# Optimization experiments

Hardware: AMD Instinct MI355X
Metric: run time of the kernel (lower is better)

The kernel has to match this reference:

```python
import jax, jax.numpy as jnp
import numpy as np

HIDDEN = 1024
N_EXPERTS = 16
TOP_K = 2
D_FF_EXPERT = 512
D_FF_SHARED = 2048
BATCH, SEQ = 1, 4096


def setup_inputs() -> dict:
    key = jax.random.key(0)
    ks = jax.random.split(key, 8)
    s = 0.02  # init scale to keep router logits sane
    return {
        "x": jax.random.normal(ks[0], (BATCH, SEQ, HIDDEN), dtype=jnp.float32),
        "router_w": jax.random.normal(ks[1], (HIDDEN, N_EXPERTS), dtype=jnp.float32) * s,
        "experts_gate": jax.random.normal(ks[2], (N_EXPERTS, HIDDEN, D_FF_EXPERT), dtype=jnp.float32) * s,
        "experts_up": jax.random.normal(ks[3], (N_EXPERTS, HIDDEN, D_FF_EXPERT), dtype=jnp.float32) * s,
        "experts_down": jax.random.normal(ks[4], (N_EXPERTS, D_FF_EXPERT, HIDDEN), dtype=jnp.float32) * s,
        "shared_gate": jax.random.normal(ks[5], (HIDDEN, D_FF_SHARED), dtype=jnp.float32) * s,
        "shared_up": jax.random.normal(ks[6], (HIDDEN, D_FF_SHARED), dtype=jnp.float32) * s,
        "shared_down": jax.random.normal(ks[7], (D_FF_SHARED, HIDDEN), dtype=jnp.float32) * s,
    }


def reference(x, router_w, experts_gate, experts_up, experts_down,
              shared_gate, shared_up, shared_down):
    B, S, D = x.shape
    T = B * S
    E = experts_gate.shape[0]

    # Shared SwiGLU expert on all tokens: silu(x@Wg) * (x@Wu) @ Wd
    shared_out = (jax.nn.silu(x @ shared_gate) * (x @ shared_up)) @ shared_down  # [B,S,D]

    x_flat = x.reshape(T, D)
    router_probs = jax.nn.softmax(x_flat @ router_w, axis=-1)          # [T,E]
    topk_w, topk_idx = jax.lax.top_k(router_probs, TOP_K)              # [T,k]

    # Combine weights as dense [T,E]; top-k indices are distinct per token,
    # exactly reproducing sum_{i in topk} w_i * expert_i(x).
    combine = jnp.zeros((T, E), x.dtype).at[jnp.arange(T)[:, None], topk_idx].add(topk_w)

    # Per-expert SwiGLU, vectorized over the (small, fixed) expert axis.
    gate = jnp.einsum('td,edf->etf', x_flat, experts_gate)             # [E,T,f]
    up = jnp.einsum('td,edf->etf', x_flat, experts_up)                 # [E,T,f]
    inter = jax.nn.silu(gate) * up                                     # [E,T,f]
    routed = jnp.einsum('etf,efd,te->td', inter, experts_down, combine)  # [T,D]

    return (shared_out.reshape(T, D) + routed).reshape(B, S, D)
```

## Files before the change

kernel.cpp:

```cpp
#include <hip/hip_runtime.h>
#include <hip/hip_bf16.h>
#include <stdint.h>

#define HIDDEN 1024
#define NEXP 16
#define DFF_E 512
#define DFF_S 2048
#define TOKENS 4096
#define NSLOTS 8192

typedef __bf16 bf16x8 __attribute__((ext_vector_type(8)));
typedef float f32x4 __attribute__((ext_vector_type(4)));

__device__ __forceinline__ unsigned short f2bf(float f) {
  unsigned int u = __builtin_bit_cast(unsigned int, f);
  u += 0x7FFFu + ((u >> 16) & 1u);
  return (unsigned short)(u >> 16);
}
__device__ __forceinline__ float bf2f(unsigned short h) {
  unsigned int u = ((unsigned int)h) << 16;
  return __builtin_bit_cast(float, u);
}
__device__ __forceinline__ void gload16(const void* g, void* l) {
  __builtin_amdgcn_global_load_lds(
      (const __attribute__((address_space(1))) unsigned int*)g,
      (__attribute__((address_space(3))) unsigned int*)l, 16, 0, 0);
}

__global__ void router_kernel(const float* __restrict__ x, const float* __restrict__ rw,
                              int* __restrict__ topk_idx, float* __restrict__ topk_w,
                              int* __restrict__ counts) {
  const int t = blockIdx.x;
  const int lane = threadIdx.x;
  float acc[NEXP];
#pragma unroll
  for (int e = 0; e < NEXP; e++) acc[e] = 0.f;
  const float* xr = x + (size_t)t * HIDDEN;
  for (int d = lane; d < HIDDEN; d += 64) {
    const float xv = xr[d];
    const float4* r = (const float4*)(rw + (size_t)d * NEXP);
#pragma unroll
    for (int q = 0; q < 4; q++) {
      float4 rv = r[q];
      acc[q * 4 + 0] += xv * rv.x;
      acc[q * 4 + 1] += xv * rv.y;
      acc[q * 4 + 2] += xv * rv.z;
      acc[q * 4 + 3] += xv * rv.w;
    }
  }
#pragma unroll
  for (int off = 32; off >= 1; off >>= 1)
#pragma unroll
    for (int e = 0; e < NEXP; e++) acc[e] += __shfl_xor(acc[e], off);

  if (lane == 0) {
    float m = acc[0];
#pragma unroll
    for (int e = 1; e < NEXP; e++) m = fmaxf(m, acc[e]);
    float p[NEXP];
    float s = 0.f;
#pragma unroll
    for (int e = 0; e < NEXP; e++) { p[e] = __expf(acc[e] - m); s += p[e]; }
    const float inv = 1.f / s;
    int i0 = 0; float p0 = p[0];
#pragma unroll
    for (int e = 1; e < NEXP; e++) if (p[e] > p0) { p0 = p[e]; i0 = e; }
    int i1 = -1; float p1 = -1.f;
#pragma unroll
    for (int e = 0; e < NEXP; e++) if (e != i0 && p[e] > p1) { p1 = p[e]; i1 = e; }
    topk_idx[t * 2 + 0] = i0;
    topk_idx[t * 2 + 1] = i1;
    topk_w[t * 2 + 0] = p0 * inv;
    topk_w[t * 2 + 1] = p1 * inv;
    atomicAdd(&counts[i0], 1);
    atomicAdd(&counts[i1], 1);
  }
}

__global__ void offsets_kernel(const int* __restrict__ counts, int* __restrict__ offs,
                               int* __restrict__ cursors) {
  if (threadIdx.x == 0) {
    int run = 0;
    for (int e = 0; e < NEXP; e++) { offs[e] = run; run += counts[e]; }
    offs[NEXP] = run;
  }
  if (threadIdx.x < NEXP) cursors[threadIdx.x] = 0;
}

__global__ void build_slots_kernel(const int* __restrict__ topk_idx, const float* __restrict__ topk_w,
                                   const int* __restrict__ offs, int* __restrict__ cursors,
                                   int* __restrict__ slot_token, float* __restrict__ slot_w,
                                   int* __restrict__ slot_pos) {
  const int t = blockIdx.x * blockDim.x + threadIdx.x;
  if (t >= TOKENS) return;
#pragma unroll
  for (int i = 0; i < 2; i++) {
    const int e = topk_idx[t * 2 + i];
    const int pos = atomicAdd(&cursors[e], 1);
    const int slot = offs[e] + pos;
    slot_token[slot] = t;
    slot_w[slot] = topk_w[t * 2 + i];
    slot_pos[t * 2 + i] = slot;
  }
}

__global__ void convert_kernel(const float* __restrict__ in, unsigned short* __restrict__ out, int n) {
  const int i = (blockIdx.x * blockDim.x + threadIdx.x) * 4;
  if (i >= n) return;
  const float4 v = *(const float4*)(in + i);
  ushort4 o;
  o.x = f2bf(v.x); o.y = f2bf(v.y); o.z = f2bf(v.z); o.w = f2bf(v.w);
  *(ushort4*)(out + i) = o;
}

__global__ void transpose_convert_kernel(const float* __restrict__ in, unsigned short* __restrict__ out,
                                         int K, int N) {
  __shared__ float tile[32][33];
  const int b = blockIdx.z;
  const int k0 = blockIdx.x * 32, n0 = blockIdx.y * 32;
  const float* src = in + (size_t)b * K * N;
  unsigned short* dst = out + (size_t)b * K * N;
  const int tx = threadIdx.x & 31, ty = threadIdx.x >> 5;
#pragma unroll
  for (int r = 0; r < 32; r += 8)
    tile[ty + r][tx] = src[(size_t)(k0 + ty + r) * N + n0 + tx];
  __syncthreads();
#pragma unroll
  for (int r = 0; r < 32; r += 8)
    dst[(size_t)(n0 + ty + r) * K + k0 + tx] = f2bf(tile[tx][ty + r]);
}

template <int GATHER>
__global__ __launch_bounds__(256) void fused_gu_k(const unsigned short* __restrict__ A,
                                                  const unsigned short* __restrict__ Bg,
                                                  const unsigned short* __restrict__ Bu,
                                                  unsigned short* __restrict__ C,
                                                  int M, int N, int K,
                                                  const int* __restrict__ offs,
                                                  const int* __restrict__ slot_token,
                                                  const float* __restrict__ slot_w) {
  __shared__ __align__(16) unsigned short As[128 * 32];
  __shared__ __align__(16) unsigned short Bgs[128 * 32];
  __shared__ __align__(16) unsigned short Bus[128 * 32];
  const int tid = threadIdx.x;
  const int lane = tid & 63;
  const int wid = tid >> 6;
  const int wr = wid >> 1, wc = wid & 1;
  const int fr = lane & 15, fq = lane >> 4;

  int rowBase, rowEnd;
  const unsigned short* Bgp = Bg;
  const unsigned short* Bup = Bu;
  if constexpr (GATHER) {
    const int e = blockIdx.z;
    const int o0 = offs[e], o1 = offs[e + 1];
    rowBase = o0 + blockIdx.x * 128;
    if (rowBase >= o1) return;
    rowEnd = o1;
    Bgp += (size_t)e * (size_t)N * (size_t)K;
    Bup += (size_t)e * (size_t)N * (size_t)K;
  } else {
    rowBase = blockIdx.x * 128;
    rowEnd = M;
  }
  const int colBase = blockIdx.y * 128;

  const int rA = tid >> 2;
  const int kOff = (tid & 3) * 8;
  const unsigned short *aRow0, *aRow1;
  {
    const int r0 = rowBase + rA, r1 = rowBase + rA + 64;
    if constexpr (GATHER) {
      const int s0 = r0 < NSLOTS ? r0 : NSLOTS - 1;
      const int s1 = r1 < NSLOTS ? r1 : NSLOTS - 1;
      aRow0 = A + (size_t)slot_token[s0] * (size_t)K;
      aRow1 = A + (size_t)slot_token[s1] * (size_t)K;
    } else {
      const int m0 = r0 < M ? r0 : M - 1;
      const int m1 = r1 < M ? r1 : M - 1;
      aRow0 = A + (size_t)m0 * (size_t)K;
      aRow1 = A + (size_t)m1 * (size_t)K;
    }
  }
  const unsigned short* bgRow0 = Bgp + (size_t)(colBase + rA) * (size_t)K;
  const unsigned short* bgRow1 = Bgp + (size_t)(colBase + rA + 64) * (size_t)K;
  const unsigned short* buRow0 = Bup + (size_t)(colBase + rA) * (size_t)K;
  const unsigned short* buRow1 = Bup + (size_t)(colBase + rA + 64) * (size_t)K;

  f32x4 accg[4][4], accu[4][4];
#pragma unroll
  for (int i = 0; i < 4; i++)
#pragma unroll
    for (int j = 0; j < 4; j++) {
      accg[i][j] = (f32x4){0.f, 0.f, 0.f, 0.f};
      accu[i][j] = (f32x4){0.f, 0.f, 0.f, 0.f};
    }

  const unsigned short* AsR = As + (wr * 64 + fr) * 32 + fq * 8;
  const unsigned short* BgsR = Bgs + (wc * 64 + fr) * 32 + fq * 8;
  const unsigned short* BusR = Bus + (wc * 64 + fr) * 32 + fq * 8;

  for (int k0 = 0; k0 < K; k0 += 32) {
    __syncthreads();
    gload16(aRow0 + k0 + kOff, As + tid * 8);
    gload16(aRow1 + k0 + kOff, As + 2048 + tid * 8);
    gload16(bgRow0 + k0 + kOff, Bgs + tid * 8);
    gload16(bgRow1 + k0 + kOff, Bgs + 2048 + tid * 8);
    gload16(buRow0 + k0 + kOff, Bus + tid * 8);
    gload16(buRow1 + k0 + kOff, Bus + 2048 + tid * 8);
    __syncthreads();
    bf16x8 af[4], bgf[4], buf[4];
#pragma unroll
    for (int m = 0; m < 4; m++) af[m] = *(const bf16x8*)(AsR + m * 512);
#pragma unroll
    for (int n = 0; n < 4; n++) bgf[n] = *(const bf16x8*)(BgsR + n * 512);
#pragma unroll
    for (int n = 0; n < 4; n++) buf[n] = *(const bf16x8*)(BusR + n * 512);
#pragma unroll
    for (int m = 0; m < 4; m++)
#pragma unroll
      for (int n = 0; n < 4; n++) {
        accg[m][n] = __builtin_amdgcn_mfma_f32_16x16x32_bf16(af[m], bgf[n], accg[m][n], 0, 0, 0);
        accu[m][n] = __builtin_amdgcn_mfma_f32_16x16x32_bf16(af[m], buf[n], accu[m][n], 0, 0, 0);
      }
  }

#pragma unroll
  for (int m = 0; m < 4; m++) {
    const int rb = rowBase + wr * 64 + m * 16 + fq * 4;
#pragma unroll
    for (int n = 0; n < 4; n++) {
      const int col = colBase + wc * 64 + n * 16 + fr;
#pragma unroll
      for (int j = 0; j < 4; j++) {
        const int r = rb + j;
        if constexpr (GATHER) {
          if (r >= rowEnd) continue;
        }
        const float g = accg[m][n][j];
        const float u = accu[m][n][j];
        float v = g / (1.f + __expf(-g)) * u;
        if constexpr (GATHER) v *= slot_w[r];
        C[(size_t)r * N + col] = f2bf(v);
      }
    }
  }
}

template <int EXPERT>
__global__ __launch_bounds__(256) void down_gemm_k(const unsigned short* __restrict__ A,
                                                   const unsigned short* __restrict__ B,
                                                   void* __restrict__ Cp, int M, int N, int K,
                                                   const int* __restrict__ offs) {
  __shared__ __align__(16) unsigned short As[128 * 32];
  __shared__ __align__(16) unsigned short Bs[128 * 32];
  const int tid = threadIdx.x;
  const int lane = tid & 63;
  const int wid = tid >> 6;
  const int wr = wid >> 1, wc = wid & 1;
  const int fr = lane & 15, fq = lane >> 4;

  int rowBase, rowEnd;
  const unsigned short* Bp = B;
  if constexpr (EXPERT) {
    const int e = blockIdx.z;
    const int o0 = offs[e], o1 = offs[e + 1];
    rowBase = o0 + blockIdx.x * 128;
    if (rowBase >= o1) return;
    rowEnd = o1;
    Bp += (size_t)e * (size_t)N * (size_t)K;
  } else {
    rowBase = blockIdx.x * 128;
    rowEnd = M;
  }
  const int colBase = blockIdx.y * 128;

  const int rA = tid >> 2;
  const int kOff = (tid & 3) * 8;
  const int maxRow = (EXPERT ? NSLOTS : M) - 1;
  const int r0 = min(rowBase + rA, maxRow);
  const int r1 = min(rowBase + rA + 64, maxRow);
  const unsigned short* aRow0 = A + (size_t)r0 * (size_t)K;
  const unsigned short* aRow1 = A + (size_t)r1 * (size_t)K;
  const unsigned short* bRow0 = Bp + (size_t)(colBase + rA) * (size_t)K;
  const unsigned short* bRow1 = Bp + (size_t)(colBase + rA + 64) * (size_t)K;

  f32x4 acc[4][4];
#pragma unroll
  for (int i = 0; i < 4; i++)
#pragma unroll
    for (int j = 0; j < 4; j++) acc[i][j] = (f32x4){0.f, 0.f, 0.f, 0.f};

  const unsigned short* AsR = As + (wr * 64 + fr) * 32 + fq * 8;
  const unsigned short* BsR = Bs + (wc * 64 + fr) * 32 + fq * 8;

  for (int k0 = 0; k0 < K; k0 += 32) {
    __syncthreads();
    gload16(aRow0 + k0 + kOff, As + tid * 8);
    gload16(aRow1 + k0 + kOff, As + 2048 + tid * 8);
    gload16(bRow0 + k0 + kOff, Bs + tid * 8);
    gload16(bRow1 + k0 + kOff, Bs + 2048 + tid * 8);
    __syncthreads();
    bf16x8 af[4], bfr[4];
#pragma unroll
    for (int m = 0; m < 4; m++) af[m] = *(const bf16x8*)(AsR + m * 512);
#pragma unroll
    for (int n = 0; n < 4; n++) bfr[n] = *(const bf16x8*)(BsR + n * 512);
#pragma unroll
    for (int m = 0; m < 4; m++)
#pragma unroll
      for (int n = 0; n < 4; n++)
        acc[m][n] = __builtin_amdgcn_mfma_f32_16x16x32_bf16(af[m], bfr[n], acc[m][n], 0, 0, 0);
  }

#pragma unroll
  for (int m = 0; m < 4; m++) {
    const int rb = rowBase + wr * 64 + m * 16 + fq * 4;
#pragma unroll
    for (int n = 0; n < 4; n++) {
      const int col = colBase + wc * 64 + n * 16 + fr;
#pragma unroll
      for (int j = 0; j < 4; j++) {
        const int r = rb + j;
        if constexpr (EXPERT) {
          if (r >= rowEnd) continue;
          ((unsigned short*)Cp)[(size_t)r * N + col] = f2bf(acc[m][n][j]);
        } else {
          ((float*)Cp)[(size_t)r * N + col] = acc[m][n][j];
        }
      }
    }
  }
}

__global__ void combine_kernel(float* __restrict__ out, const unsigned short* __restrict__ dslot,
                               const int* __restrict__ slot_pos) {
  const int t = blockIdx.x;
  const int s0 = slot_pos[t * 2 + 0];
  const int s1 = slot_pos[t * 2 + 1];
  const int c = threadIdx.x * 4;
  const ushort4 a = *(const ushort4*)(dslot + (size_t)s0 * HIDDEN + c);
  const ushort4 b = *(const ushort4*)(dslot + (size_t)s1 * HIDDEN + c);
  float4* o = (float4*)(out + (size_t)t * HIDDEN + c);
  float4 v = *o;
  v.x += bf2f(a.x) + bf2f(b.x);
  v.y += bf2f(a.y) + bf2f(b.y);
  v.z += bf2f(a.z) + bf2f(b.z);
  v.w += bf2f(a.w) + bf2f(b.w);
  *o = v;
}

#define WS_XB 0ull
#define WS_WEG 8388608ull
#define WS_WEU 25165824ull
#define WS_WED 41943040ull
#define WS_WSG 58720256ull
#define WS_WSU 62914560ull
#define WS_WSD 67108864ull
#define WS_INTERB 71303168ull
#define WS_INTERS 88080384ull
#define WS_DSLOT 96468992ull
#define WS_SLOT_TOKEN 113246208ull
#define WS_SLOT_W 113278976ull
#define WS_SLOT_POS 113311744ull
#define WS_TOPK_IDX 113344512ull
#define WS_TOPK_W 113377280ull
#define WS_COUNTS 113410048ull
#define WS_OFFS 113410112ull
#define WS_CURSORS 113410240ull
#define WS_NEEDED 113410304ull

extern "C" void kernel_launch(void* const* d_in, const int* in_sizes, int n_in,
                              void* d_out, int out_size, void* d_ws, size_t ws_size,
                              hipStream_t stream) {
  if (ws_size < WS_NEEDED) return;

  const float* x = (const float*)d_in[0];
  const float* router_w = (const float*)d_in[1];
  const float* eg = (const float*)d_in[2];
  const float* eu = (const float*)d_in[3];
  const float* ed = (const float*)d_in[4];
  const float* sg = (const float*)d_in[5];
  const float* su = (const float*)d_in[6];
  const float* sd = (const float*)d_in[7];

  char* ws = (char*)d_ws;
  unsigned short* xb = (unsigned short*)(ws + WS_XB);
  unsigned short* weg = (unsigned short*)(ws + WS_WEG);
  unsigned short* weu = (unsigned short*)(ws + WS_WEU);
  unsigned short* wed = (unsigned short*)(ws + WS_WED);
  unsigned short* wsg = (unsigned short*)(ws + WS_WSG);
  unsigned short* wsu = (unsigned short*)(ws + WS_WSU);
  unsigned short* wsd = (unsigned short*)(ws + WS_WSD);
  unsigned short* interb = (unsigned short*)(ws + WS_INTERB);
  unsigned short* inters = (unsigned short*)(ws + WS_INTERS);
  unsigned short* dslot = (unsigned short*)(ws + WS_DSLOT);
  int* slot_token = (int*)(ws + WS_SLOT_TOKEN);
  float* slot_w = (float*)(ws + WS_SLOT_W);
  int* slot_pos = (int*)(ws + WS_SLOT_POS);
  int* topk_idx = (int*)(ws + WS_TOPK_IDX);
  float* topk_w = (float*)(ws + WS_TOPK_W);
  int* counts = (int*)(ws + WS_COUNTS);
  int* offs = (int*)(ws + WS_OFFS);
  int* cursors = (int*)(ws + WS_CURSORS);

  float* out = (float*)d_out;

  hipMemsetAsync(counts, 0, NEXP * sizeof(int), stream);
  router_kernel<<<TOKENS, 64, 0, stream>>>(x, router_w, topk_idx, topk_w, counts);
  offsets_kernel<<<1, 64, 0, stream>>>(counts, offs, cursors);
  build_slots_kernel<<<16, 256, 0, stream>>>(topk_idx, topk_w, offs, cursors,
                                             slot_token, slot_w, slot_pos);

  convert_kernel<<<4096, 256, 0, stream>>>(x, xb, TOKENS * HIDDEN);
  transpose_convert_kernel<<<dim3(32, 16, 16), 256, 0, stream>>>(eg, weg, 1024, 512);
  transpose_convert_kernel<<<dim3(32, 16, 16), 256, 0, stream>>>(eu, weu, 1024, 512);
  transpose_convert_kernel<<<dim3(16, 32, 16), 256, 0, stream>>>(ed, wed, 512, 1024);
  transpose_convert_kernel<<<dim3(32, 64, 1), 256, 0, stream>>>(sg, wsg, 1024, 2048);
  transpose_convert_kernel<<<dim3(32, 64, 1), 256, 0, stream>>>(su, wsu, 1024, 2048);
  transpose_convert_kernel<<<dim3(64, 32, 1), 256, 0, stream>>>(sd, wsd, 2048, 1024);

  fused_gu_k<0><<<dim3(32, 16, 1), 256, 0, stream>>>(xb, wsg, wsu, interb, TOKENS, DFF_S, HIDDEN,
                                                     nullptr, nullptr, nullptr);
  down_gemm_k<0><<<dim3(32, 8, 1), 256, 0, stream>>>(interb, wsd, out, TOKENS, HIDDEN, DFF_S, nullptr);

  fused_gu_k<1><<<dim3(16, 4, 16), 256, 0, stream>>>(xb, weg, weu, inters, NSLOTS, DFF_E, HIDDEN,
                                                     offs, slot_token, slot_w);
  down_gemm_k<1><<<dim3(16, 8, 16), 256, 0, stream>>>(inters, wed, dslot, NSLOTS, HIDDEN, DFF_E, offs);
  combine_kernel<<<TOKENS, 256, 0, stream>>>(out, dslot, slot_pos);
}
```

Baseline: 684.9 us.

## Double-buffer LDS tiles in MoE GEMM kernels to overlap global loads with MFMA

Both the fused gate/up GEMM and the down GEMM now use two LDS buffers per operand. The next K-slice is prefetched with global_load_lds while MFMAs run on the current slice, and each step ends with explicit waitcnt plus a barrier. This hides global memory latency that the old load-sync-compute loop exposed. LDS use doubles, which may lower occupancy, and the correctness of the hand-placed waitcnts depends on compiler scheduling.

```diff
diff --git a/kernel.cpp b/kernel.cpp
--- a/kernel.cpp
+++ b/kernel.cpp
@@ -25,6 +25,17 @@
   __builtin_amdgcn_global_load_lds(
       (const __attribute__((address_space(1))) unsigned int*)g,
       (__attribute__((address_space(3))) unsigned int*)l, 16, 0, 0);
+}
+__device__ __forceinline__ void wait_vmcnt0() {
+  asm volatile("s_waitcnt vmcnt(0)" ::: "memory");
+}
+__device__ __forceinline__ void wait_lgkmcnt0() {
+  asm volatile("s_waitcnt lgkmcnt(0)" ::: "memory");
+}
+__device__ __forceinline__ void hard_barrier() {
+  __builtin_amdgcn_sched_barrier(0);
+  __builtin_amdgcn_s_barrier();
+  __builtin_amdgcn_sched_barrier(0);
 }
 
 __global__ void router_kernel(const float* __restrict__ x, const float* __restrict__ rw,
@@ -139,9 +150,9 @@
                                                   const int* __restrict__ offs,
                                                   const int* __restrict__ slot_token,
                                                   const float* __restrict__ slot_w) {
-  __shared__ __align__(16) unsigned short As[128 * 32];
-  __shared__ __align__(16) unsigned short Bgs[128 * 32];
-  __shared__ __align__(16) unsigned short Bus[128 * 32];
+  __shared__ __align__(16) unsigned short As[2][4096];
+  __shared__ __align__(16) unsigned short Bgs[2][4096];
+  __shared__ __align__(16) unsigned short Bus[2][4096];
   const int tid = threadIdx.x;
   const int lane = tid & 63;
   const int wid = tid >> 6;
@@ -196,33 +207,46 @@
       accu[i][j] = (f32x4){0.f, 0.f, 0.f, 0.f};
     }
 
-  const unsigned short* AsR = As + (wr * 64 + fr) * 32 + fq * 8;
-  const unsigned short* BgsR = Bgs + (wc * 64 + fr) * 32 + fq * 8;
-  const unsigned short* BusR = Bus + (wc * 64 + fr) * 32 + fq * 8;
-
-  for (int k0 = 0; k0 < K; k0 += 32) {
-    __syncthreads();
-    gload16(aRow0 + k0 + kOff, As + tid * 8);
-    gload16(aRow1 + k0 + kOff, As + 2048 + tid * 8);
-    gload16(bgRow0 + k0 + kOff, Bgs + tid * 8);
-    gload16(bgRow1 + k0 + kOff, Bgs + 2048 + tid * 8);
-    gload16(buRow0 + k0 + kOff, Bus + tid * 8);
-    gload16(buRow1 + k0 + kOff, Bus + 2048 + tid * 8);
-    __syncthreads();
-    bf16x8 af[4], bgf[4], buf[4];
-#pragma unroll
-    for (int m = 0; m < 4; m++) af[m] = *(const bf16x8*)(AsR + m * 512);
-#pragma unroll
-    for (int n = 0; n < 4; n++) bgf[n] = *(const bf16x8*)(BgsR + n * 512);
-#pragma unroll
-    for (int n = 0; n < 4; n++) buf[n] = *(const bf16x8*)(BusR + n * 512);
+  const int ldOff = tid * 8;
+  auto stage = [&](int b, int k0) {
+    gload16(aRow0 + k0 + kOff, &As[b][ldOff]);
+    gload16(aRow1 + k0 + kOff, &As[b][2048 + ldOff]);
+    gload16(bgRow0 + k0 + kOff, &Bgs[b][ldOff]);
+    gload16(bgRow1 + k0 + kOff, &Bgs[b][2048 + ldOff]);
+    gload16(buRow0 + k0 + kOff, &Bus[b][ldOff]);
+    gload16(buRow1 + k0 + kOff, &Bus[b][2048 + ldOff]);
+  };
+
+  const int rdA = (wr * 64 + fr) * 32 + fq * 8;
+  const int rdB = (wc * 64 + fr) * 32 + fq * 8;
+
+  const int nsteps = K >> 5;
+  int cur = 0;
+  stage(0, 0);
+  wait_vmcnt0();
+  hard_barrier();
+
+  for (int s = 0; s < nsteps; ++s) {
+    if (s + 1 < nsteps) stage(cur ^ 1, (s + 1) << 5);
+    bf16x8 af[4], bgf[4], buf_[4];
+#pragma unroll
+    for (int m = 0; m < 4; m++) af[m] = *(const bf16x8*)(&As[cur][rdA + m * 512]);
+#pragma unroll
+    for (int n = 0; n < 4; n++) bgf[n] = *(const bf16x8*)(&Bgs[cur][rdB + n * 512]);
+#pragma unroll
+    for (int n = 0; n < 4; n++) buf_[n] = *(const bf16x8*)(&Bus[cur][rdB + n * 512]);
+    wait_lgkmcnt0();
+    __builtin_amdgcn_sched_barrier(0);
 #pragma unroll
     for (int m = 0; m < 4; m++)
 #pragma unroll
       for (int n = 0; n < 4; n++) {
         accg[m][n] = __builtin_amdgcn_mfma_f32_16x16x32_bf16(af[m], bgf[n], accg[m][n], 0, 0, 0);
-        accu[m][n] = __builtin_amdgcn_mfma_f32_16x16x32_bf16(af[m], buf[n], accu[m][n], 0, 0, 0);
+        accu[m][n] = __builtin_amdgcn_mfma_f32_16x16x32_bf16(af[m], buf_[n], accu[m][n], 0, 0, 0);
       }
+    wait_vmcnt0();
+    hard_barrier();
+    cur ^= 1;
   }
 
 #pragma unroll
@@ -252,8 +276,8 @@
                                                    const unsigned short* __restrict__ B,
                                                    void* __restrict__ Cp, int M, int N, int K,
                                                    const int* __restrict__ offs) {
-  __shared__ __align__(16) unsigned short As[128 * 32];
-  __shared__ __align__(16) unsigned short Bs[128 * 32];
+  __shared__ __align__(16) unsigned short As[2][4096];
+  __shared__ __align__(16) unsigned short Bs[2][4096];
   const int tid = threadIdx.x;
   const int lane = tid & 63;
   const int wid = tid >> 6;
@@ -291,26 +315,40 @@
 #pragma unroll
     for (int j = 0; j < 4; j++) acc[i][j] = (f32x4){0.f, 0.f, 0.f, 0.f};
 
-  const unsigned short* AsR = As + (wr * 64 + fr) * 32 + fq * 8;
-  const unsigned short* BsR = Bs + (wc * 64 + fr) * 32 + fq * 8;
-
-  for (int k0 = 0; k0 < K; k0 += 32) {
-    __syncthreads();
-    gload16(aRow0 + k0 + kOff, As + tid * 8);
-    gload16(aRow1 + k0 + kOff, As + 2048 + tid * 8);
-    gload16(bRow0 + k0 + kOff, Bs + tid * 8);
-    gload16(bRow1 + k0 + kOff, Bs + 2048 + tid * 8);
-    __syncthreads();
+  const int ldOff = tid * 8;
+  auto stage = [&](int b, int k0) {
+    gload16(aRow0 + k0 + kOff, &As[b][ldOff]);
+    gload16(aRow1 + k0 + kOff, &As[b][2048 + ldOff]);
+    gload16(bRow0 + k0 + kOff, &Bs[b][ldOff]);
+    gload16(bRow1 + k0 + kOff, &Bs[b][2048 + ldOff]);
+  };
+
+  const int rdA = (wr * 64 + fr) * 32 + fq * 8;
+  const int rdB = (wc * 64 + fr) * 32 + fq * 8;
+
+  const int nsteps = K >> 5;
+  int cur = 0;
+  stage(0, 0);
+  wait_vmcnt0();
+  hard_barrier();
+
+  for (int s = 0; s < nsteps; ++s) {
+    if (s + 1 < nsteps) stage(cur ^ 1, (s + 1) << 5);
     bf16x8 af[4], bfr[4];
 #pragma unroll
-    for (int m = 0; m < 4; m++) af[m] = *(const bf16x8*)(AsR + m * 512);
-#pragma unroll
-    for (int n = 0; n < 4; n++) bfr[n] = *(const bf16x8*)(BsR + n * 512);
+    for (int m = 0; m < 4; m++) af[m] = *(const bf16x8*)(&As[cur][rdA + m * 512]);
+#pragma unroll
+    for (int n = 0; n < 4; n++) bfr[n] = *(const bf16x8*)(&Bs[cur][rdB + n * 512]);
+    wait_lgkmcnt0();
+    __builtin_amdgcn_sched_barrier(0);
 #pragma unroll
     for (int m = 0; m < 4; m++)
 #pragma unroll
       for (int n = 0; n < 4; n++)
         acc[m][n] = __builtin_amdgcn_mfma_f32_16x16x32_bf16(af[m], bfr[n], acc[m][n], 0, 0, 0);
+    wait_vmcnt0();
+    hard_barrier();
+    cur ^= 1;
   }
 
 #pragma unroll
```

After: 644.3 us. 1.06x faster.
